# Performance work log

Measured on AMD Instinct MI355X. Metric: run time of the kernel, lower is better.

## Reference

```python
import jax, jax.numpy as jnp
import numpy as np


def setup_inputs() -> dict:
    key = jax.random.key(0)
    B, n = 1048576, 8
    x = jax.random.normal(key, (B, n, n), dtype=jnp.float32)
    return {"x": x, "num_iters": 5}


def reference(x, num_iters):
    # FusedMHC.forward: flatten to [B, n, n] in fp32, run Sinkhorn, cast back.
    input_dtype = x.dtype
    n = x.shape[-1]
    M = jnp.exp(x.reshape(-1, n, n).astype(jnp.float32))  # positive kernel matrix
    # num_iters alternating row / column normalizations (Sinkhorn-Knopp)
    for _ in range(num_iters):
        M = M / jnp.sum(M, axis=-1, keepdims=True)  # row normalize
        M = M / jnp.sum(M, axis=-2, keepdims=True)  # col normalize
    return M.reshape(x.shape).astype(input_dtype)
```

## Files before the change

### kernel.cpp

```cpp
#include <hip/hip_runtime.h>


#define N 8

__global__ __launch_bounds__(256) void sinkhorn8_kernel(
    const float* __restrict__ x,
    float* __restrict__ out,
    const int* __restrict__ num_iters_p,
    int B)
{
    int tid = blockIdx.x * blockDim.x + threadIdx.x;
    int m = tid >> 4;
    if (m >= B) return;

    const int num_iters = *num_iters_p;

    float4 v = ((const float4*)x)[tid];

    v.x = __expf(v.x);
    v.y = __expf(v.y);
    v.z = __expf(v.z);
    v.w = __expf(v.w);

    for (int it = 0; it < num_iters; ++it) {
        float rs = v.x + v.y + v.z + v.w;
        rs += __shfl_xor(rs, 1, 64);
        float rinv = __builtin_amdgcn_rcpf(rs);
        v.x *= rinv;
        v.y *= rinv;
        v.z *= rinv;
        v.w *= rinv;

        float4 cs = v;
#pragma unroll
        for (int d = 2; d <= 8; d <<= 1) {
            cs.x += __shfl_xor(cs.x, d, 64);
            cs.y += __shfl_xor(cs.y, d, 64);
            cs.z += __shfl_xor(cs.z, d, 64);
            cs.w += __shfl_xor(cs.w, d, 64);
        }
        v.x *= __builtin_amdgcn_rcpf(cs.x);
        v.y *= __builtin_amdgcn_rcpf(cs.y);
        v.z *= __builtin_amdgcn_rcpf(cs.z);
        v.w *= __builtin_amdgcn_rcpf(cs.w);
    }

    ((float4*)out)[tid] = v;
}

extern "C" void kernel_launch(void* const* d_in, const int* in_sizes, int n_in,
                              void* d_out, int out_size, void* d_ws, size_t ws_size,
                              hipStream_t stream) {
    const float* x = (const float*)d_in[0];
    const int* num_iters = (const int*)d_in[1];
    float* out = (float*)d_out;

    int B = in_sizes[0] / (N * N);
    long long total_threads = (long long)B * 16;
    int block = 256;
    long long grid = (total_threads + block - 1) / block;

    sinkhorn8_kernel<<<(int)grid, block, 0, stream>>>(x, out, num_iters, B);
}
```

Baseline: 482.8 us.

## Remap lanes so column reductions use DPP quad_perm and row_ror

Each lane of a 16-lane group now maps to a different (row, half) pair, so the three column-sum butterfly steps land on lane distances that DPP can express: quad_perm swaps and a row rotate by 8. This replaces ds_bpermute-based shuffles with DPP moves inside the VALU, which avoids LDS-path latency inside the iteration loop. The row pair now sits at lane distance 4 and still uses a shuffle. Memory accesses within each matrix become slightly permuted but stay within the same 256-byte span.

```diff
diff --git a/kernel.cpp b/kernel.cpp
--- a/kernel.cpp
+++ b/kernel.cpp
@@ -2,6 +2,12 @@
 
 
 #define N 8
+
+template <int CTRL>
+__device__ __forceinline__ float dpp_xor(float x) {
+    int r = __builtin_amdgcn_update_dpp(0, __float_as_int(x), CTRL, 0xF, 0xF, true);
+    return __int_as_float(r);
+}
 
 __global__ __launch_bounds__(256) void sinkhorn8_kernel(
     const float* __restrict__ x,
@@ -15,7 +21,12 @@
 
     const int num_iters = *num_iters_p;
 
-    float4 v = ((const float4*)x)[tid];
+    int t = tid & 15;
+    int row = (t & 3) | ((t >> 1) & 4);
+    int h = (t >> 2) & 1;
+    size_t idx = ((size_t)m << 4) + (size_t)(row * 2 + h);
+
+    float4 v = ((const float4*)x)[idx];
 
     v.x = __expf(v.x);
     v.y = __expf(v.y);
@@ -24,7 +35,7 @@
 
     for (int it = 0; it < num_iters; ++it) {
         float rs = v.x + v.y + v.z + v.w;
-        rs += __shfl_xor(rs, 1, 64);
+        rs += __shfl_xor(rs, 4, 64);
         float rinv = __builtin_amdgcn_rcpf(rs);
         v.x *= rinv;
         v.y *= rinv;
@@ -32,20 +43,28 @@
         v.w *= rinv;
 
         float4 cs = v;
-#pragma unroll
-        for (int d = 2; d <= 8; d <<= 1) {
-            cs.x += __shfl_xor(cs.x, d, 64);
-            cs.y += __shfl_xor(cs.y, d, 64);
-            cs.z += __shfl_xor(cs.z, d, 64);
-            cs.w += __shfl_xor(cs.w, d, 64);
-        }
+        cs.x += dpp_xor<0xB1>(cs.x);
+        cs.y += dpp_xor<0xB1>(cs.y);
+        cs.z += dpp_xor<0xB1>(cs.z);
+        cs.w += dpp_xor<0xB1>(cs.w);
+
+        cs.x += dpp_xor<0x4E>(cs.x);
+        cs.y += dpp_xor<0x4E>(cs.y);
+        cs.z += dpp_xor<0x4E>(cs.z);
+        cs.w += dpp_xor<0x4E>(cs.w);
+
+        cs.x += dpp_xor<0x128>(cs.x);
+        cs.y += dpp_xor<0x128>(cs.y);
+        cs.z += dpp_xor<0x128>(cs.z);
+        cs.w += dpp_xor<0x128>(cs.w);
+
         v.x *= __builtin_amdgcn_rcpf(cs.x);
         v.y *= __builtin_amdgcn_rcpf(cs.y);
         v.z *= __builtin_amdgcn_rcpf(cs.z);
         v.w *= __builtin_amdgcn_rcpf(cs.w);
     }
 
-    ((float4*)out)[tid] = v;
+    ((float4*)out)[idx] = v;
 }
 
 extern "C" void kernel_launch(void* const* d_in, const int* in_sizes, int n_in,
```

After: 411.7 us. -14.7%, faster.
